# Kernel tuning notes

Hardware: AMD Instinct MI355X
Metric: run time of the kernel (lower is better)

The kernel has to match this reference:

```python
import jax, jax.numpy as jnp
import numpy as np

B, P, N = 64, 100, 1000
EMB, H, D = 256, 16, 16  # head_num*qkv_dim == EMB
CTX = 4 * EMB            # len(node_schedule)+1 = 4 context levels
SQRT_EMB = 16.0
CLIP = 10.0


def setup_inputs() -> dict:
    key = jax.random.key(0)
    ks = jax.random.split(key, 10)
    s = 0.02
    return {
        "encoded_last_node": jax.random.normal(ks[0], (B, P, EMB), jnp.float32),
        "attr": jax.random.uniform(ks[1], (B, P, 4), jnp.float32),
        "multi_level_context": jax.random.normal(ks[2], (B, CTX), jnp.float32),
        "ninf_mask": jnp.zeros((B, P, N), jnp.float32),
        "encoded_nodes": jax.random.normal(ks[3], (B, N, EMB), jnp.float32),
        "Wq_last": jax.random.normal(ks[4], (EMB + 4 + CTX, H * D), jnp.float32) * s,
        "Wk": jax.random.normal(ks[5], (EMB, H * D), jnp.float32) * s,
        "Wv": jax.random.normal(ks[6], (EMB, H * D), jnp.float32) * s,
        "Wcomb": jax.random.normal(ks[7], (H * D, EMB), jnp.float32) * s,
        "bcomb": jnp.zeros((EMB,), jnp.float32),
    }


def _heads(x):  # [B, n, H*D] -> [B, H, n, D]
    b, n, _ = x.shape
    return x.reshape(b, n, H, D).transpose(0, 2, 1, 3)


def reference(encoded_last_node, attr, multi_level_context, ninf_mask,
              encoded_nodes, Wq_last, Wk, Wv, Wcomb, bcomb):
    # set_kv
    k = _heads(encoded_nodes @ Wk)          # [B,H,N,D]
    v = _heads(encoded_nodes @ Wv)          # [B,H,N,D]
    single_head_key = encoded_nodes         # used as [B,EMB,N] via einsum

    # query from last node + attrs + broadcast multi-level context
    ctx = jnp.broadcast_to(multi_level_context[:, None, :], (B, P, CTX))
    input_cat = jnp.concatenate([encoded_last_node, attr, ctx], axis=2)
    q = _heads(input_cat @ Wq_last)         # [B,H,P,D]

    # masked multi-head attention
    score = jnp.einsum('bhpd,bhnd->bhpn', q, k) / jnp.sqrt(jnp.float32(D))
    score = score + ninf_mask[:, None, :, :]
    w = jax.nn.softmax(score, axis=3)
    out = jnp.einsum('bhpn,bhnd->bhpd', w, v)           # [B,H,P,D]
    out_concat = out.transpose(0, 2, 1, 3).reshape(B, P, H * D)

    # combine (Linear branch; num_experts == 1)
    mh = out_concat @ Wcomb + bcomb                     # [B,P,EMB]

    # single-head pointer logits with tanh clipping
    s = jnp.einsum('bpe,bne->bpn', mh, single_head_key) / SQRT_EMB
    s = CLIP * jnp.tanh(s) + ninf_mask
    probs = jax.nn.softmax(s, axis=2)
    return probs
```

## Files before the change

kernel.cpp:

```cpp
#include <hip/hip_runtime.h>
#include <hip/hip_bf16.h>
#include <math.h>

#define B_  64
#define P_  100
#define N_  1000
#define EMB_ 256
#define H_  16
#define D_  16
#define CTX_ 1024
#define L2E 1.44269504088896340736f

#if __has_builtin(__builtin_amdgcn_exp2f)
#define EXP2F(x) __builtin_amdgcn_exp2f(x)
#else
#define EXP2F(x) exp2f(x)
#endif

typedef __bf16 bf16_t;
typedef bf16_t bf16x8 __attribute__((ext_vector_type(8)));
typedef bf16_t bf16x4 __attribute__((ext_vector_type(4)));
typedef float  f32x4  __attribute__((ext_vector_type(4)));
typedef short  s16x4  __attribute__((ext_vector_type(4)));

#if __has_builtin(__builtin_amdgcn_mfma_f32_16x16x16bf16_1k)
__device__ __forceinline__ void pv_mfma16(bf16x4 a, bf16x4 b, f32x4& c)
{
    s16x4 ai, bi;
    __builtin_memcpy(&ai, &a, 8);
    __builtin_memcpy(&bi, &b, 8);
    c = __builtin_amdgcn_mfma_f32_16x16x16bf16_1k(ai, bi, c, 0, 0, 0);
}
__device__ __forceinline__ void mfma_hazard_fence() {}
#else
__device__ __forceinline__ void pv_mfma16(bf16x4 a, bf16x4 b, f32x4& c)
{
    asm("s_nop 1\n\tv_mfma_f32_16x16x16_bf16 %0, %1, %2, %0"
        : "+v"(c) : "v"(a), "v"(b));
}
__device__ __forceinline__ void mfma_hazard_fence()
{
    __builtin_amdgcn_sched_barrier(0);
    asm volatile("s_nop 7\n\ts_nop 3");
}
#endif

__device__ __forceinline__ bf16x8 ldcvt8(const float* __restrict__ p)
{
    float4 u = *(const float4*)p;
    float4 v = *(const float4*)(p + 4);
    bf16x8 r;
    r[0] = (bf16_t)u.x; r[1] = (bf16_t)u.y; r[2] = (bf16_t)u.z; r[3] = (bf16_t)u.w;
    r[4] = (bf16_t)v.x; r[5] = (bf16_t)v.y; r[6] = (bf16_t)v.z; r[7] = (bf16_t)v.w;
    return r;
}

__global__ __launch_bounds__(256) void wtrans_kernel(
    const float* __restrict__ W0, const float* __restrict__ W1,
    const float* __restrict__ W2, const float* __restrict__ W3,
    bf16_t* __restrict__ T0, bf16_t* __restrict__ T1,
    bf16_t* __restrict__ T2, bf16_t* __restrict__ T3)
{
    __shared__ float t[32][33];
    const float* W = (blockIdx.z == 0) ? W0 : (blockIdx.z == 1) ? W1
                   : (blockIdx.z == 2) ? W2 : W3;
    bf16_t*      T = (blockIdx.z == 0) ? T0 : (blockIdx.z == 1) ? T1
                   : (blockIdx.z == 2) ? T2 : T3;
    const int n0 = blockIdx.x * 32, k0 = blockIdx.y * 32;
    const int tx = threadIdx.x & 31, ty = threadIdx.x >> 5;
#pragma unroll
    for (int i = 0; i < 4; ++i)
        t[ty + i * 8][tx] = W[(size_t)(k0 + ty + i * 8) * 256 + n0 + tx];
    __syncthreads();
#pragma unroll
    for (int i = 0; i < 4; ++i)
        T[(size_t)(n0 + ty + i * 8) * 256 + k0 + tx] = (bf16_t)t[tx][ty + i * 8];
}

template<bool BIAS, bool OUT_BF16>
__global__ __launch_bounds__(256) void mfma_gemm(
    const bf16_t* __restrict__ A, const bf16_t* __restrict__ BT,
    const float* __restrict__ bias, void* __restrict__ Cout)
{
    const int wave = threadIdx.x >> 6;
    const int lane = threadIdx.x & 63;
    const int m0 = blockIdx.x * 16;
    const int n0 = wave * 64;
    const int lr = lane & 15;
    const int lk = (lane >> 4) * 8;

    const bf16_t* ap = A  + (size_t)(m0 + lr) * 256 + lk;
    const bf16_t* bp = BT + (size_t)(n0 + lr) * 256 + lk;

    f32x4 acc[4];
#pragma unroll
    for (int j = 0; j < 4; ++j) acc[j] = (f32x4)0.f;

#pragma unroll 2
    for (int k0 = 0; k0 < 256; k0 += 32) {
        bf16x8 a = *(const bf16x8*)(ap + k0);
#pragma unroll
        for (int j = 0; j < 4; ++j) {
            bf16x8 b = *(const bf16x8*)(bp + (size_t)j * 16 * 256 + k0);
            acc[j] = __builtin_amdgcn_mfma_f32_16x16x32_bf16(a, b, acc[j], 0, 0, 0);
        }
    }

    const int crow = m0 + (lane >> 4) * 4;
#pragma unroll
    for (int j = 0; j < 4; ++j) {
        const int col = n0 + j * 16 + lr;
        const float bv = BIAS ? bias[col] : 0.f;
#pragma unroll
        for (int r = 0; r < 4; ++r) {
            float val = acc[j][r] + bv;
            if (OUT_BF16)
                ((bf16_t*)Cout)[(size_t)(crow + r) * 256 + col] = (bf16_t)val;
            else
                ((float*)Cout)[(size_t)(crow + r) * 256 + col] = val;
        }
    }
}

__global__ __launch_bounds__(256) void mfma_gemm_q(
    const float* __restrict__ A, const bf16_t* __restrict__ BT,
    const float* __restrict__ qcpart, const float* __restrict__ attr,
    const float* __restrict__ Wq, float* __restrict__ Cout)
{
    const int wave = threadIdx.x >> 6;
    const int lane = threadIdx.x & 63;
    const int m0 = blockIdx.x * 16;
    const int n0 = wave * 64;
    const int lr = lane & 15;
    const int lk = (lane >> 4) * 8;

    const float*  ap = A  + (size_t)(m0 + lr) * 256 + lk;
    const bf16_t* bp = BT + (size_t)(n0 + lr) * 256 + lk;

    f32x4 acc[4];
#pragma unroll
    for (int j = 0; j < 4; ++j) acc[j] = (f32x4)0.f;

#pragma unroll 2
    for (int k0 = 0; k0 < 256; k0 += 32) {
        bf16x8 a = ldcvt8(ap + k0);
#pragma unroll
        for (int j = 0; j < 4; ++j) {
            bf16x8 b = *(const bf16x8*)(bp + (size_t)j * 16 * 256 + k0);
            acc[j] = __builtin_amdgcn_mfma_f32_16x16x32_bf16(a, b, acc[j], 0, 0, 0);
        }
    }

    const int crow = m0 + (lane >> 4) * 4;
#pragma unroll
    for (int j = 0; j < 4; ++j) {
        const int col = n0 + j * 16 + lr;
#pragma unroll
        for (int r = 0; r < 4; ++r) {
            const int row = crow + r;
            const int b = row / P_;
            float add = 0.f;
#pragma unroll
            for (int kc = 0; kc < 4; ++kc)
                add += qcpart[((size_t)kc * 64 + b) * EMB_ + col];
            add = fmaf(attr[(size_t)row * 4 + 0], Wq[(size_t)256 * EMB_ + col], add);
            add = fmaf(attr[(size_t)row * 4 + 1], Wq[(size_t)257 * EMB_ + col], add);
            add = fmaf(attr[(size_t)row * 4 + 2], Wq[(size_t)258 * EMB_ + col], add);
            add = fmaf(attr[(size_t)row * 4 + 3], Wq[(size_t)259 * EMB_ + col], add);
            Cout[(size_t)row * 256 + col] = acc[j][r] + add;
        }
    }
}

__global__ __launch_bounds__(256) void mfma_gemm_kv(
    const float* __restrict__ A, const bf16_t* __restrict__ BTk,
    const bf16_t* __restrict__ BTv,
    bf16_t* __restrict__ Ck, bf16_t* __restrict__ Cv,
    bf16_t* __restrict__ nbf)
{
    const int wave = threadIdx.x >> 6;
    const int lane = threadIdx.x & 63;
    const int m0 = blockIdx.x * 64;
    const int n0 = wave * 64;
    const int lr = lane & 15;
    const int lk = (lane >> 4) * 8;

    const float* ap[4];
    bf16_t* np[4];
#pragma unroll
    for (int m = 0; m < 4; ++m) {
        ap[m] = A   + (size_t)(m0 + m * 16 + lr) * 256 + lk;
        np[m] = nbf + (size_t)(m0 + m * 16 + lr) * 256 + lk;
    }
    const bf16_t* bpk = BTk + (size_t)(n0 + lr) * 256 + lk;
    const bf16_t* bpv = BTv + (size_t)(n0 + lr) * 256 + lk;

    f32x4 acck[4][4], accv[4][4];
#pragma unroll
    for (int m = 0; m < 4; ++m)
#pragma unroll
        for (int j = 0; j < 4; ++j) { acck[m][j] = (f32x4)0.f; accv[m][j] = (f32x4)0.f; }

    for (int k0 = 0; k0 < 256; k0 += 32) {
        bf16x8 a0 = ldcvt8(ap[0] + k0);
        bf16x8 a1 = ldcvt8(ap[1] + k0);
        bf16x8 a2 = ldcvt8(ap[2] + k0);
        bf16x8 a3 = ldcvt8(ap[3] + k0);
        if (wave == 0) {
            *(bf16x8*)(np[0] + k0) = a0;
            *(bf16x8*)(np[1] + k0) = a1;
            *(bf16x8*)(np[2] + k0) = a2;
            *(bf16x8*)(np[3] + k0) = a3;
        }
#pragma unroll
        for (int j = 0; j < 4; ++j) {
            bf16x8 bk = *(const bf16x8*)(bpk + (size_t)j * 16 * 256 + k0);
            bf16x8 bv = *(const bf16x8*)(bpv + (size_t)j * 16 * 256 + k0);
            acck[0][j] = __builtin_amdgcn_mfma_f32_16x16x32_bf16(bk, a0, acck[0][j], 0, 0, 0);
            acck[1][j] = __builtin_amdgcn_mfma_f32_16x16x32_bf16(bk, a1, acck[1][j], 0, 0, 0);
            acck[2][j] = __builtin_amdgcn_mfma_f32_16x16x32_bf16(bk, a2, acck[2][j], 0, 0, 0);
            acck[3][j] = __builtin_amdgcn_mfma_f32_16x16x32_bf16(bk, a3, acck[3][j], 0, 0, 0);
            accv[0][j] = __builtin_amdgcn_mfma_f32_16x16x32_bf16(bv, a0, accv[0][j], 0, 0, 0);
            accv[1][j] = __builtin_amdgcn_mfma_f32_16x16x32_bf16(bv, a1, accv[1][j], 0, 0, 0);
            accv[2][j] = __builtin_amdgcn_mfma_f32_16x16x32_bf16(bv, a2, accv[2][j], 0, 0, 0);
            accv[3][j] = __builtin_amdgcn_mfma_f32_16x16x32_bf16(bv, a3, accv[3][j], 0, 0, 0);
        }
    }

    const int lg4 = (lane >> 4) * 4;
#pragma unroll
    for (int m = 0; m < 4; ++m) {
        const size_t rowoff = (size_t)(m0 + m * 16 + lr) * 256;
#pragma unroll
        for (int j = 0; j < 4; ++j) {
            const int col = n0 + j * 16 + lg4;
            bf16x4 ok, ov;
#pragma unroll
            for (int r = 0; r < 4; ++r) {
                ok[r] = (bf16_t)acck[m][j][r];
                ov[r] = (bf16_t)accv[m][j][r];
            }
            *(bf16x4*)(Ck + rowoff + col) = ok;
            *(bf16x4*)(Cv + rowoff + col) = ov;
        }
    }
}

__global__ __launch_bounds__(256) void qc_kernel(
    const float* __restrict__ ctx, const float* __restrict__ Wq,
    float* __restrict__ qcpart)
{
    const int b = blockIdx.x;
    const int kc = blockIdx.y;
    const int tid = threadIdx.x;
    const float* c = ctx + (size_t)b * CTX_ + kc * 256;
    const float* w = Wq + (size_t)(260 + kc * 256) * EMB_ + tid;
    float acc = 0.f;
#pragma unroll 8
    for (int kk = 0; kk < 256; ++kk)
        acc = fmaf(c[kk], w[(size_t)kk * EMB_], acc);
    qcpart[((size_t)kc * 64 + b) * EMB_ + tid] = acc;
}

struct AttnState { float m, l; f32x4 acc; };

template<bool TAIL>
__device__ __forceinline__ void attn_chunk(
    int n0, const bf16_t* __restrict__ kb, const bf16_t* __restrict__ vb,
    const float* __restrict__ maskrow, bf16x8 qfrag, int lr, int lg,
    AttnState& st)
{
    int nk = n0 + lr;
    if (TAIL) nk = (nk < N_) ? nk : (N_ - 1);
    bf16x8 ak = *(const bf16x8*)(kb + (size_t)nk * 256 + (lg & 1) * 8);
    if (lg >= 2) ak = (bf16x8)(bf16_t)0.0f;

    f32x4 sc = __builtin_amdgcn_mfma_f32_16x16x32_bf16(ak, qfrag, (f32x4)0.f, 0, 0, 0);

    int nm = n0 + 4 * lg;
    if (TAIL) nm = (nm < 996) ? nm : 996;
    float4 mk = *(const float4*)&maskrow[nm];
    float s0 = fmaf(sc[0], 0.25f, mk.x);
    float s1 = fmaf(sc[1], 0.25f, mk.y);
    float s2 = fmaf(sc[2], 0.25f, mk.z);
    float s3 = fmaf(sc[3], 0.25f, mk.w);
    if (TAIL) {
        if (n0 + 4 * lg + 0 >= N_) s0 = -3.0e38f;
        if (n0 + 4 * lg + 1 >= N_) s1 = -3.0e38f;
        if (n0 + 4 * lg + 2 >= N_) s2 = -3.0e38f;
        if (n0 + 4 * lg + 3 >= N_) s3 = -3.0e38f;
    }

    float tmax = fmaxf(fmaxf(s0, s1), fmaxf(s2, s3));
    if (__any(tmax > st.m + 8.0f)) {
        float rmax = fmaxf(tmax, __shfl_xor(tmax, 16));
        rmax = fmaxf(rmax, __shfl_xor(rmax, 32));
        float mn = fmaxf(st.m, rmax);
        mfma_hazard_fence();
        float f = EXP2F((st.m - mn) * L2E);
        st.l *= f;
        st.acc *= f;
        st.m = mn;
    }
    float w0 = EXP2F((s0 - st.m) * L2E);
    float w1 = EXP2F((s1 - st.m) * L2E);
    float w2 = EXP2F((s2 - st.m) * L2E);
    float w3 = EXP2F((s3 - st.m) * L2E);
    st.l += (w0 + w1) + (w2 + w3);
    bf16x4 pb;
    pb[0] = (bf16_t)w0; pb[1] = (bf16_t)w1; pb[2] = (bf16_t)w2; pb[3] = (bf16_t)w3;

    bf16x4 av;
#pragma unroll
    for (int i = 0; i < 4; ++i) {
        int nn = n0 + 4 * lg + i;
        if (TAIL) nn = (nn < N_) ? nn : (N_ - 1);
        av[i] = vb[(size_t)nn * 256 + lr];
    }
    pv_mfma16(av, pb, st.acc);
}

__global__ __launch_bounds__(1024) void attn_mfma(
    const float* __restrict__ q, const bf16_t* __restrict__ k,
    const bf16_t* __restrict__ v, const float* __restrict__ mask,
    bf16_t* __restrict__ abuf)
{
    const int x = blockIdx.x;
    const int xcd = x & 7;
    const int slot = x >> 3;
    const int b = xcd + 8 * (slot / 7);
    const int mtile = slot % 7;
    const int h = threadIdx.x >> 6;
    const int lane = threadIdx.x & 63;
    const int p0 = mtile * 16;
    const int lr = lane & 15;
    const int lg = lane >> 4;

    const int pq = (p0 + lr < P_) ? (p0 + lr) : (P_ - 1);
    bf16x8 qfrag = (bf16x8)(bf16_t)0.0f;
    if (lg < 2) {
        const float* qp = q + ((size_t)b * P_ + pq) * 256 + h * 16 + lg * 8;
        float4 q0 = *(const float4*)qp;
        float4 q1 = *(const float4*)(qp + 4);
        qfrag[0] = (bf16_t)q0.x; qfrag[1] = (bf16_t)q0.y;
        qfrag[2] = (bf16_t)q0.z; qfrag[3] = (bf16_t)q0.w;
        qfrag[4] = (bf16_t)q1.x; qfrag[5] = (bf16_t)q1.y;
        qfrag[6] = (bf16_t)q1.z; qfrag[7] = (bf16_t)q1.w;
    }

    const bf16_t* kb = k + ((size_t)b * N_) * 256 + h * 16;
    const bf16_t* vb = v + ((size_t)b * N_) * 256 + h * 16;
    const float* maskrow = mask + ((size_t)b * P_ + pq) * N_;

    AttnState stA, stB;
    stA.m = -INFINITY; stA.l = 0.f; stA.acc = (f32x4)0.f;
    stB.m = -INFINITY; stB.l = 0.f; stB.acc = (f32x4)0.f;

    for (int n0 = 0; n0 < 960; n0 += 32) {
        attn_chunk<false>(n0,      kb, vb, maskrow, qfrag, lr, lg, stA);
        attn_chunk<false>(n0 + 16, kb, vb, maskrow, qfrag, lr, lg, stB);
    }
    attn_chunk<false>(960, kb, vb, maskrow, qfrag, lr, lg, stA);
    attn_chunk<false>(976, kb, vb, maskrow, qfrag, lr, lg, stB);
    attn_chunk<true>(992, kb, vb, maskrow, qfrag, lr, lg, stA);

    mfma_hazard_fence();
    float mn = fmaxf(stA.m, stB.m);
    float fA = EXP2F((stA.m - mn) * L2E);
    float fB = EXP2F((stB.m - mn) * L2E);
    float l = stA.l * fA + stB.l * fB;
    f32x4 acc = stA.acc * fA + stB.acc * fB;

    float L = l + __shfl_xor(l, 16);
    L += __shfl_xor(L, 32);

    if (p0 + lr < P_) {
        float inv = 1.0f / L;
        bf16x4 o;
        o[0] = (bf16_t)(acc[0] * inv);
        o[1] = (bf16_t)(acc[1] * inv);
        o[2] = (bf16_t)(acc[2] * inv);
        o[3] = (bf16_t)(acc[3] * inv);
        *(bf16x4*)(abuf + ((size_t)b * P_ + p0 + lr) * 256 + h * 16 + 4 * lg) = o;
    }
}

__global__ __launch_bounds__(1024) void logits_softmax(
    const bf16_t* __restrict__ mh, const bf16_t* __restrict__ nodes,
    const float* __restrict__ mask, float* __restrict__ out)
{
    __shared__ float redm[16][16];
    __shared__ float reds[16][16];

    const int x = blockIdx.x;
    const int xcd = x & 7;
    const int slot = x >> 3;
    const int b = xcd + 8 * (slot / 7);
    const int mt = slot % 7;
    const int wave = threadIdx.x >> 6;
    const int lane = threadIdx.x & 63;
    const int p0 = mt * 16;
    const int n0 = wave * 64;
    const int lr = lane & 15;
    const int lg = lane >> 4;
    const int lk = lg * 8;

    const bf16_t* bbase = nodes + (size_t)b * N_ * 256;
    int nrow[4];
#pragma unroll
    for (int j = 0; j < 4; ++j) {
        int n = n0 + j * 16 + lr;
        nrow[j] = (n < N_) ? n : (N_ - 1);
    }
    const bf16_t* ap = mh + ((size_t)(b * P_) + p0 + lr) * 256 + lk;

    f32x4 acc[4];
#pragma unroll
    for (int j = 0; j < 4; ++j) acc[j] = (f32x4)0.f;

#pragma unroll 2
    for (int k0 = 0; k0 < 256; k0 += 32) {
        bf16x8 a = *(const bf16x8*)(ap + k0);
#pragma unroll
        for (int j = 0; j < 4; ++j) {
            bf16x8 bfr = *(const bf16x8*)(bbase + (size_t)nrow[j] * 256 + lk + k0);
            acc[j] = __builtin_amdgcn_mfma_f32_16x16x32_bf16(a, bfr, acc[j], 0, 0, 0);
        }
    }

    const int prowb = p0 + lg * 4;
    float lv[4][4];
#pragma unroll
    for (int j = 0; j < 4; ++j) {
        const int n = n0 + j * 16 + lr;
        const int nc = (n < N_) ? n : (N_ - 1);
#pragma unroll
        for (int r = 0; r < 4; ++r) {
            const int p = prowb + r;
            const int pc = (p < P_) ? p : (P_ - 1);
            float xv = acc[j][r] * (1.0f / 16.0f);
            float e = EXP2F(xv * (2.0f * L2E));
            float t = 1.0f - 2.0f / (e + 1.0f);
            float val = 10.0f * t + mask[((size_t)(b * P_ + pc)) * N_ + nc];
            lv[j][r] = (n < N_) ? val : -3.0e38f;
        }
    }

    float pm[4];
#pragma unroll
    for (int r = 0; r < 4; ++r) {
        pm[r] = fmaxf(fmaxf(lv[0][r], lv[1][r]), fmaxf(lv[2][r], lv[3][r]));
        pm[r] = fmaxf(pm[r], __shfl_xor(pm[r], 1));
        pm[r] = fmaxf(pm[r], __shfl_xor(pm[r], 2));
        pm[r] = fmaxf(pm[r], __shfl_xor(pm[r], 4));
        pm[r] = fmaxf(pm[r], __shfl_xor(pm[r], 8));
    }
    if (lr == 0) {
#pragma unroll
        for (int r = 0; r < 4; ++r) redm[wave][lg * 4 + r] = pm[r];
    }
    __syncthreads();
    float gm[4];
#pragma unroll
    for (int r = 0; r < 4; ++r) {
        float m_ = redm[0][lg * 4 + r];
#pragma unroll
        for (int w = 1; w < 16; ++w) m_ = fmaxf(m_, redm[w][lg * 4 + r]);
        gm[r] = m_;
    }

    float ps[4];
#pragma unroll
    for (int r = 0; r < 4; ++r) ps[r] = 0.f;
#pragma unroll
    for (int j = 0; j < 4; ++j)
#pragma unroll
        for (int r = 0; r < 4; ++r) {
            float e = EXP2F((lv[j][r] - gm[r]) * L2E);
            lv[j][r] = e;
            ps[r] += e;
        }
#pragma unroll
    for (int r = 0; r < 4; ++r) {
        ps[r] += __shfl_xor(ps[r], 1);
        ps[r] += __shfl_xor(ps[r], 2);
        ps[r] += __shfl_xor(ps[r], 4);
        ps[r] += __shfl_xor(ps[r], 8);
    }
    if (lr == 0) {
#pragma unroll
        for (int r = 0; r < 4; ++r) reds[wave][lg * 4 + r] = ps[r];
    }
    __syncthreads();
    float inv[4];
#pragma unroll
    for (int r = 0; r < 4; ++r) {
        float s = 0.f;
#pragma unroll
        for (int w = 0; w < 16; ++w) s += reds[w][lg * 4 + r];
        inv[r] = 1.0f / s;
    }

#pragma unroll
    for (int j = 0; j < 4; ++j) {
        const int n = n0 + j * 16 + lr;
        if (n >= N_) continue;
#pragma unroll
        for (int r = 0; r < 4; ++r) {
            const int p = prowb + r;
            if (p >= P_) continue;
            out[((size_t)(b * P_ + p)) * N_ + n] = lv[j][r] * inv[r];
        }
    }
}

extern "C" void kernel_launch(void* const* d_in, const int* in_sizes, int n_in,
                              void* d_out, int out_size, void* d_ws, size_t ws_size,
                              hipStream_t stream)
{
    const float* lastnode = (const float*)d_in[0];
    const float* attr     = (const float*)d_in[1];
    const float* ctx      = (const float*)d_in[2];
    const float* mask     = (const float*)d_in[3];
    const float* nodes    = (const float*)d_in[4];
    const float* Wq       = (const float*)d_in[5];
    const float* Wk       = (const float*)d_in[6];
    const float* Wv       = (const float*)d_in[7];
    const float* Wcomb    = (const float*)d_in[8];
    const float* bcomb    = (const float*)d_in[9];
    float* out = (float*)d_out;

    float* ws = (float*)d_ws;
    bf16_t* kbuf   = (bf16_t*)(ws);
    bf16_t* vbuf   = (bf16_t*)(ws + 8192000);
    float*  qbuf   = ws + 16384000;
    bf16_t* nbf    = (bf16_t*)(ws + 18022400);
    bf16_t* WkT    = (bf16_t*)(ws + 26214400);
    bf16_t* WvT    = (bf16_t*)(ws + 26247168);
    bf16_t* WcombT = (bf16_t*)(ws + 26279936);
    bf16_t* WqmT   = (bf16_t*)(ws + 26312704);
    float*  qcpart = ws + 26345472;
    bf16_t* abuf   = (bf16_t*)(ws + 26411008);
    bf16_t* mhbuf = kbuf;

    wtrans_kernel<<<dim3(8, 8, 4), 256, 0, stream>>>(
        Wk, Wv, Wcomb, Wq, WkT, WvT, WcombT, WqmT);

    qc_kernel<<<dim3(64, 4), 256, 0, stream>>>(ctx, Wq, qcpart);
    mfma_gemm_q<<<400, 256, 0, stream>>>(lastnode, WqmT, qcpart, attr, Wq, qbuf);

    mfma_gemm_kv<<<1000, 256, 0, stream>>>(nodes, WkT, WvT, kbuf, vbuf, nbf);

    attn_mfma<<<448, 1024, 0, stream>>>(qbuf, kbuf, vbuf, mask, abuf);

    mfma_gemm<true, true><<<400, 256, 0, stream>>>(abuf, WcombT, bcomb, mhbuf);

    logits_softmax<<<448, 1024, 0, stream>>>(mhbuf, nbf, mask, out);
}
```

Before: 277.1 us.

## Stage K/V tiles through double-buffered LDS in attention kernel

```diff
diff --git a/kernel.cpp b/kernel.cpp
--- a/kernel.cpp
+++ b/kernel.cpp
@@ -10,6 +10,7 @@
 #define D_  16
 #define CTX_ 1024
 #define L2E 1.44269504088896340736f
+#define LROW 264
 
 #if __has_builtin(__builtin_amdgcn_exp2f)
 #define EXP2F(x) __builtin_amdgcn_exp2f(x)
@@ -265,14 +266,12 @@
 struct AttnState { float m, l; f32x4 acc; };
 
 template<bool TAIL>
-__device__ __forceinline__ void attn_chunk(
-    int n0, const bf16_t* __restrict__ kb, const bf16_t* __restrict__ vb,
-    const float* __restrict__ maskrow, bf16x8 qfrag, int lr, int lg,
+__device__ __forceinline__ void attn_chunk_lds(
+    int n0, const bf16_t* __restrict__ skb, const bf16_t* __restrict__ svb,
+    const float* __restrict__ maskrow, bf16x8 qfrag, int h, int lr, int lg,
     AttnState& st)
 {
-    int nk = n0 + lr;
-    if (TAIL) nk = (nk < N_) ? nk : (N_ - 1);
-    bf16x8 ak = *(const bf16x8*)(kb + (size_t)nk * 256 + (lg & 1) * 8);
+    bf16x8 ak = *(const bf16x8*)(skb + lr * LROW + h * 16 + (lg & 1) * 8);
     if (lg >= 2) ak = (bf16x8)(bf16_t)0.0f;
 
     f32x4 sc = __builtin_amdgcn_mfma_f32_16x16x32_bf16(ak, qfrag, (f32x4)0.f, 0, 0, 0);
@@ -312,11 +311,8 @@
 
     bf16x4 av;
 #pragma unroll
-    for (int i = 0; i < 4; ++i) {
-        int nn = n0 + 4 * lg + i;
-        if (TAIL) nn = (nn < N_) ? nn : (N_ - 1);
-        av[i] = vb[(size_t)nn * 256 + lr];
-    }
+    for (int i = 0; i < 4; ++i)
+        av[i] = svb[(4 * lg + i) * LROW + h * 16 + lr];
     pv_mfma16(av, pb, st.acc);
 }
 
@@ -325,6 +321,9 @@
     const bf16_t* __restrict__ v, const float* __restrict__ mask,
     bf16_t* __restrict__ abuf)
 {
+    __shared__ bf16_t sk[2][16][LROW];
+    __shared__ bf16_t sv[2][16][LROW];
+
     const int x = blockIdx.x;
     const int xcd = x & 7;
     const int slot = x >> 3;
@@ -336,6 +335,12 @@
     const int lr = lane & 15;
     const int lg = lane >> 4;
 
+    const int tid = threadIdx.x;
+    const int sh  = tid >> 9;
+    const int t2  = tid & 511;
+    const int srow = t2 >> 5;
+    const int scol = (t2 & 31) * 8;
+
     const int pq = (p0 + lr < P_) ? (p0 + lr) : (P_ - 1);
     bf16x8 qfrag = (bf16x8)(bf16_t)0.0f;
     if (lg < 2) {
@@ -348,21 +353,40 @@
         qfrag[6] = (bf16_t)q1.z; qfrag[7] = (bf16_t)q1.w;
     }
 
-    const bf16_t* kb = k + ((size_t)b * N_) * 256 + h * 16;
-    const bf16_t* vb = v + ((size_t)b * N_) * 256 + h * 16;
+    const bf16_t* kfull = k + (size_t)b * N_ * 256;
+    const bf16_t* vfull = v + (size_t)b * N_ * 256;
+    const bf16_t* sbase = sh ? vfull : kfull;
     const float* maskrow = mask + ((size_t)b * P_ + pq) * N_;
 
     AttnState stA, stB;
     stA.m = -INFINITY; stA.l = 0.f; stA.acc = (f32x4)0.f;
     stB.m = -INFINITY; stB.l = 0.f; stB.acc = (f32x4)0.f;
 
-    for (int n0 = 0; n0 < 960; n0 += 32) {
-        attn_chunk<false>(n0,      kb, vb, maskrow, qfrag, lr, lg, stA);
-        attn_chunk<false>(n0 + 16, kb, vb, maskrow, qfrag, lr, lg, stB);
-    }
-    attn_chunk<false>(960, kb, vb, maskrow, qfrag, lr, lg, stA);
-    attn_chunk<false>(976, kb, vb, maskrow, qfrag, lr, lg, stB);
-    attn_chunk<true>(992, kb, vb, maskrow, qfrag, lr, lg, stA);
+    {
+        const bf16_t* src = sbase + (size_t)srow * 256 + scol;
+        bf16_t* dst = sh ? &sv[0][srow][scol] : &sk[0][srow][scol];
+        *(bf16x8*)dst = *(const bf16x8*)src;
+    }
+    __syncthreads();
+
+    for (int it = 0; it < 62; ++it) {
+        {
+            const int rr = min((it + 1) * 16 + srow, N_ - 1);
+            const bf16_t* src = sbase + (size_t)rr * 256 + scol;
+            bf16_t* dst = sh ? &sv[(it + 1) & 1][srow][scol]
+                             : &sk[(it + 1) & 1][srow][scol];
+            *(bf16x8*)dst = *(const bf16x8*)src;
+        }
+        if (it & 1)
+            attn_chunk_lds<false>(it * 16, &sk[it & 1][0][0], &sv[it & 1][0][0],
+                                  maskrow, qfrag, h, lr, lg, stB);
+        else
+            attn_chunk_lds<false>(it * 16, &sk[it & 1][0][0], &sv[it & 1][0][0],
+                                  maskrow, qfrag, h, lr, lg, stA);
+        __syncthreads();
+    }
+    attn_chunk_lds<true>(992, &sk[0][0][0], &sv[0][0][0],
+                         maskrow, qfrag, h, lr, lg, stA);
 
     mfma_hazard_fence();
     float mn = fmaxf(stA.m, stB.m);
```

Result: faster. 250.2 us (-9.7%).
